# Kernel optimization log

Hardware: AMD Instinct MI355X
Metric: run time of the kernel (lower is better)

The kernel has to match this reference:

```python
import jax, jax.numpy as jnp
import numpy as np

N = 100000   # nodes
E = 600000   # edges
G = 4096     # graphs in batch
D_IN = 73
D_E = 101
D = 128      # latent_dim
BN_EPS = 1e-5


def _bn(h, gamma, beta):
    # BatchNorm1d in training mode: batch statistics (biased variance)
    m = h.mean(axis=0)
    v = h.var(axis=0)
    return (h - m) * jax.lax.rsqrt(v + BN_EPS) * gamma + beta


def setup_inputs() -> dict:
    key = jax.random.key(0)
    ks = jax.random.split(key, 24)
    inp = {
        "x": jax.random.normal(ks[0], (N, D_IN), jnp.float32),
        "edge_attr": jax.random.normal(ks[1], (E, D_E), jnp.float32),
        "src": jax.random.randint(ks[2], (E,), 0, N, jnp.int32),
        "dst": jax.random.randint(ks[3], (E,), 0, N, jnp.int32),
        "batch": jnp.sort(jax.random.randint(ks[4], (N,), 0, G, jnp.int32)),
        # node embedding Linear(73 -> 128)
        "W_emb": jax.random.normal(ks[5], (D_IN, D), jnp.float32) / np.sqrt(D_IN),
        "b_emb": jnp.zeros((D,), jnp.float32),
    }
    k = 6
    for i in range(2):
        inp[f"We{i}"] = jax.random.normal(ks[k], (D_E, D), jnp.float32) / np.sqrt(D_E); k += 1
        inp[f"be{i}"] = jnp.zeros((D,), jnp.float32)
        inp[f"W1_{i}"] = jax.random.normal(ks[k], (D, 2 * D), jnp.float32) / np.sqrt(D); k += 1
        inp[f"b1_{i}"] = jnp.zeros((2 * D,), jnp.float32)
        inp[f"g1_{i}"] = jnp.ones((2 * D,), jnp.float32)
        inp[f"bb1_{i}"] = jnp.zeros((2 * D,), jnp.float32)
        inp[f"W2_{i}"] = jax.random.normal(ks[k], (2 * D, D), jnp.float32) / np.sqrt(2 * D); k += 1
        inp[f"b2_{i}"] = jnp.zeros((D,), jnp.float32)
        inp[f"go_{i}"] = jnp.ones((D,), jnp.float32)
        inp[f"bo_{i}"] = jnp.zeros((D,), jnp.float32)
    return inp


def _forward(x, edge_attr, src, dst, batch,
             W_emb, b_emb,
             We0, be0, W1_0, b1_0, g1_0, bb1_0, W2_0, b2_0, go_0, bo_0,
             We1, be1, W1_1, b1_1, g1_1, bb1_1, W2_1, b2_1, go_1, bo_1):
    layers = [
        (We0, be0, W1_0, b1_0, g1_0, bb1_0, W2_0, b2_0, go_0, bo_0),
        (We1, be1, W1_1, b1_1, g1_1, bb1_1, W2_1, b2_1, go_1, bo_1),
    ]
    h = x @ W_emb + b_emb  # [N, D]
    n_layers = len(layers)
    for i, (We, be, W1, b1, g1, bb1, W2, b2, go, bo) in enumerate(layers):
        e = edge_attr @ We + be                         # [E, D]
        msg = jax.nn.relu(h[src] + e)                   # gather + add + ReLU
        agg = jax.ops.segment_sum(msg, dst, num_segments=N)  # scatter-sum
        z = h + agg                                     # (1 + eps) * x_i + aggr, eps = 0
        z = jax.nn.relu(_bn(z @ W1 + b1, g1, bb1))      # MLP: Linear -> BN -> ReLU
        h = _bn(z @ W2 + b2, go, bo)                    # Linear -> outer BN
        if i != n_layers - 1:
            h = jax.nn.relu(h)
        # dropout p=0 -> identity
    # global mean pool over graphs
    sums = jax.ops.segment_sum(h, batch, num_segments=G)            # [G, D]
    counts = jax.ops.segment_sum(jnp.ones((h.shape[0],), h.dtype), batch, num_segments=G)
    return sums / jnp.maximum(counts, 1.0)[:, None]


def reference(x, edge_attr, src, dst, batch,
              W_emb, b_emb,
              We0, be0, W1_0, b1_0, g1_0, bb1_0, W2_0, b2_0, go_0, bo_0,
              We1, be1, W1_1, b1_1, g1_1, bb1_1, W2_1, b2_1, go_1, bo_1):
    return _forward(x, edge_attr, src, dst, batch, W_emb, b_emb,
                    We0, be0, W1_0, b1_0, g1_0, bb1_0, W2_0, b2_0, go_0, bo_0,
                    We1, be1, W1_1, b1_1, g1_1, bb1_1, W2_1, b2_1, go_1, bo_1)
```

## Files before the change

### kernel.cpp

```cpp
#include <hip/hip_runtime.h>
#include <cstddef>

#define NN  100000
#define NE  600000
#define NG  4096
#define DIN 73
#define DE  101
#define DD  128
#define DD2 256
#define NP  100096
#define EP  600064

typedef unsigned int uint;
typedef unsigned short ushort;
typedef __attribute__((ext_vector_type(8))) short bf16x8;
typedef __attribute__((ext_vector_type(4))) float f32x4;

__device__ __forceinline__ void fadd_atomic(float* p, float v) { unsafeAtomicAdd(p, v); }

__device__ __forceinline__ ushort f2bf(float f) {
    uint u = __float_as_uint(f);
    uint r = (u + 0x7fffu + ((u >> 16) & 1u)) >> 16;
    return (ushort)r;
}
__device__ __forceinline__ float bf2f(ushort u) { return __uint_as_float(((uint)u) << 16); }


__global__ void hist_kernel(const int* __restrict__ dst, int* __restrict__ deg) {
    int e = blockIdx.x * blockDim.x + threadIdx.x;
    if (e < NE) atomicAdd(&deg[dst[e]], 1);
}

__global__ __launch_bounds__(256) void scan_chunk_kernel(
    const int* __restrict__ deg, int* __restrict__ offs, int* __restrict__ csums)
{
    const int b = blockIdx.x, t = threadIdx.x;
    const int base = b * 1024 + t * 4;
    int v[4];
    #pragma unroll
    for (int i = 0; i < 4; ++i) v[i] = (base + i < NN) ? deg[base + i] : 0;
    int tsum = v[0] + v[1] + v[2] + v[3];
    const int lane = t & 63, w = t >> 6;
    int x = tsum;
    #pragma unroll
    for (int d = 1; d < 64; d <<= 1) {
        int y = __shfl_up(x, d, 64);
        if (lane >= d) x += y;
    }
    __shared__ int wsum[4];
    if (lane == 63) wsum[w] = x;
    __syncthreads();
    int woff = 0;
    for (int i = 0; i < w; ++i) woff += wsum[i];
    int run = woff + x - tsum;
    #pragma unroll
    for (int i = 0; i < 4; ++i) {
        if (base + i < NN) offs[base + i] = run;
        run += v[i];
    }
    if (t == 255) csums[b] = woff + x;
}

__global__ void scan_tops_kernel(int* __restrict__ csums, int* __restrict__ offs, int nchunks) {
    if (threadIdx.x == 0 && blockIdx.x == 0) {
        int run = 0;
        for (int i = 0; i < nchunks; ++i) { int c = csums[i]; csums[i] = run; run += c; }
        offs[NN] = run;
    }
}

__global__ void scan_add_kernel(int* __restrict__ offs, const int* __restrict__ csums) {
    int i = blockIdx.x * blockDim.x + threadIdx.x;
    if (i < NN) offs[i] += csums[i >> 10];
}

__global__ void scatter_kernel(const int* __restrict__ dst, const int* __restrict__ offs,
                               int* __restrict__ cursor, int* __restrict__ csr)
{
    int e = blockIdx.x * blockDim.x + threadIdx.x;
    if (e >= NE) return;
    int d = dst[e];
    int pos = offs[d] + atomicAdd(&cursor[d], 1);
    csr[pos] = e;
}

__global__ void gstart_kernel(const int* __restrict__ batch, int* __restrict__ gstart) {
    int n = blockIdx.x * blockDim.x + threadIdx.x;
    if (n > NN) return;
    if (n == NN) {
        for (int g = batch[NN - 1] + 1; g <= NG; ++g) gstart[g] = NN;
        return;
    }
    int b = batch[n];
    int pb = (n == 0) ? -1 : batch[n - 1];
    for (int g = pb + 1; g <= b; ++g) gstart[g] = n;
}


__global__ __launch_bounds__(256) void cvt_ea_kernel(const float* __restrict__ ea,
                                                     ushort* __restrict__ eab)
{
    const int t = threadIdx.x;
    const int r = blockIdx.x * 8 + (t >> 5);
    if (r >= NE) return;
    const int c = (t & 31) * 4;
    ushort4 o;
    o.x = (c + 0 < DE) ? f2bf(ea[(size_t)r * DE + c + 0]) : (ushort)0;
    o.y = (c + 1 < DE) ? f2bf(ea[(size_t)r * DE + c + 1]) : (ushort)0;
    o.z = (c + 2 < DE) ? f2bf(ea[(size_t)r * DE + c + 2]) : (ushort)0;
    o.w = (c + 3 < DE) ? f2bf(ea[(size_t)r * DE + c + 3]) : (ushort)0;
    *(ushort4*)&eab[(size_t)r * 128 + c] = o;
}

__global__ void cvt_wt_kernel(const float* __restrict__ in, ushort* __restrict__ out,
                              int Kin, int Nn, int Kp)
{
    const int n = blockIdx.x;
    for (int k = threadIdx.x; k < Kp; k += blockDim.x)
        out[(size_t)n * Kp + k] = (k < Kin) ? f2bf(in[(size_t)k * Nn + n]) : (ushort)0;
}

template<int K>
__device__ __forceinline__ void mma_core(const ushort* __restrict__ Wt,
                                         const ushort* __restrict__ X,
                                         int n0, int m0, f32x4 acc[4][8])
{
    const int lane = threadIdx.x & 63;
    const int l15 = lane & 15, grp = lane >> 4;
    const size_t aoff = (size_t)(n0 + l15) * K + grp * 8;
    const size_t boff = (size_t)(m0 + l15) * K + grp * 8;
    #pragma unroll
    for (int kk = 0; kk < K / 32; ++kk) {
        bf16x8 a[8], b[4];
        #pragma unroll
        for (int nf = 0; nf < 8; ++nf)
            a[nf] = *(const bf16x8*)(Wt + aoff + (size_t)nf * 16 * K + kk * 32);
        #pragma unroll
        for (int mf = 0; mf < 4; ++mf)
            b[mf] = *(const bf16x8*)(X + boff + (size_t)mf * 16 * K + kk * 32);
        #pragma unroll
        for (int mf = 0; mf < 4; ++mf)
            #pragma unroll
            for (int nf = 0; nf < 8; ++nf)
                acc[mf][nf] = __builtin_amdgcn_mfma_f32_16x16x32_bf16(a[nf], b[mf], acc[mf][nf], 0, 0, 0);
    }
}

__device__ __forceinline__ void acc_zero(f32x4 acc[4][8]) {
    #pragma unroll
    for (int i = 0; i < 4; ++i)
        #pragma unroll
        for (int j = 0; j < 8; ++j)
            acc[i][j] = (f32x4){0.f, 0.f, 0.f, 0.f};
}

__global__ __launch_bounds__(256) void edge_gemm_kernel(
    const ushort* __restrict__ eab, const ushort* __restrict__ Wt,
    const float* __restrict__ be, const int* __restrict__ src,
    const float* __restrict__ h, ushort* __restrict__ msg)
{
    f32x4 acc[4][8];
    acc_zero(acc);
    const int e0 = blockIdx.x * 256 + (threadIdx.x >> 6) * 64;
    mma_core<128>(Wt, eab, 0, e0, acc);
    const int lane = threadIdx.x & 63, l15 = lane & 15, grp = lane >> 4;
    float4 bev[8];
    #pragma unroll
    for (int nf = 0; nf < 8; ++nf) bev[nf] = *(const float4*)&be[nf * 16 + grp * 4];
    #pragma unroll
    for (int mf = 0; mf < 4; ++mf) {
        const int e = e0 + mf * 16 + l15;
        const int sn = src[min(e, NE - 1)];
        const float* hp = &h[(size_t)sn * 128];
        #pragma unroll
        for (int nf = 0; nf < 8; ++nf) {
            const int nb = nf * 16 + grp * 4;
            const float4 hv = *(const float4*)&hp[nb];
            ushort4 o;
            o.x = f2bf(fmaxf(acc[mf][nf][0] + bev[nf].x + hv.x, 0.f));
            o.y = f2bf(fmaxf(acc[mf][nf][1] + bev[nf].y + hv.y, 0.f));
            o.z = f2bf(fmaxf(acc[mf][nf][2] + bev[nf].z + hv.z, 0.f));
            o.w = f2bf(fmaxf(acc[mf][nf][3] + bev[nf].w + hv.w, 0.f));
            *(ushort4*)&msg[(size_t)e * 128 + nb] = o;
        }
    }
}

__global__ __launch_bounds__(256) void mlp1_gemm_kernel(
    const ushort* __restrict__ z, const ushort* __restrict__ Wt,
    const float* __restrict__ bias, ushort* __restrict__ y)
{
    f32x4 acc[4][8];
    acc_zero(acc);
    const int m0 = blockIdx.x * 256 + (threadIdx.x >> 6) * 64;
    const int n0 = blockIdx.y * 128;
    mma_core<128>(Wt, z, n0, m0, acc);
    const int lane = threadIdx.x & 63, l15 = lane & 15, grp = lane >> 4;
    #pragma unroll
    for (int nf = 0; nf < 8; ++nf) {
        const int nb = n0 + nf * 16 + grp * 4;
        const float4 bv = *(const float4*)&bias[nb];
        #pragma unroll
        for (int mf = 0; mf < 4; ++mf) {
            const size_t m = m0 + mf * 16 + l15;
            ushort4 o;
            o.x = f2bf(acc[mf][nf][0] + bv.x);
            o.y = f2bf(acc[mf][nf][1] + bv.y);
            o.z = f2bf(acc[mf][nf][2] + bv.z);
            o.w = f2bf(acc[mf][nf][3] + bv.w);
            *(ushort4*)&y[m * 256 + nb] = o;
        }
    }
}

__global__ __launch_bounds__(256) void mlp2_gemm_kernel(
    const ushort* __restrict__ y1, const ushort* __restrict__ Wt,
    const float* __restrict__ bias, float* __restrict__ y2)
{
    f32x4 acc[4][8];
    acc_zero(acc);
    const int m0 = blockIdx.x * 256 + (threadIdx.x >> 6) * 64;
    mma_core<256>(Wt, y1, 0, m0, acc);
    const int lane = threadIdx.x & 63, l15 = lane & 15, grp = lane >> 4;
    #pragma unroll
    for (int nf = 0; nf < 8; ++nf) {
        const int nb = nf * 16 + grp * 4;
        const float4 bv = *(const float4*)&bias[nb];
        #pragma unroll
        for (int mf = 0; mf < 4; ++mf) {
            const size_t m = m0 + mf * 16 + l15;
            float4 o;
            o.x = acc[mf][nf][0] + bv.x;
            o.y = acc[mf][nf][1] + bv.y;
            o.z = acc[mf][nf][2] + bv.z;
            o.w = acc[mf][nf][3] + bv.w;
            *(float4*)&y2[m * 128 + nb] = o;
        }
    }
}


__global__ __launch_bounds__(128) void embed_kernel(
    const float* __restrict__ x, const float* __restrict__ W,
    const float* __restrict__ b, float* __restrict__ h)
{
    __shared__ float xs[4][DIN];
    const int n0 = blockIdx.x * 4;
    const int d  = threadIdx.x;
    for (int idx = d; idx < 4 * DIN; idx += 128) {
        int r = idx / DIN, c = idx - r * DIN;
        xs[r][c] = x[(size_t)n0 * DIN + idx];
    }
    __syncthreads();
    float bb = b[d];
    float a0 = bb, a1 = bb, a2 = bb, a3 = bb;
    for (int k = 0; k < DIN; ++k) {
        float w = W[k * DD + d];
        a0 = fmaf(xs[0][k], w, a0);
        a1 = fmaf(xs[1][k], w, a1);
        a2 = fmaf(xs[2][k], w, a2);
        a3 = fmaf(xs[3][k], w, a3);
    }
    h[(size_t)(n0 + 0) * DD + d] = a0;
    h[(size_t)(n0 + 1) * DD + d] = a1;
    h[(size_t)(n0 + 2) * DD + d] = a2;
    h[(size_t)(n0 + 3) * DD + d] = a3;
}

__global__ __launch_bounds__(256) void agg_kernel(
    const int* __restrict__ offs, const int* __restrict__ csr,
    const ushort* __restrict__ msgb, const float* __restrict__ h,
    ushort* __restrict__ zb)
{
    const int n = blockIdx.x * 4 + (threadIdx.x >> 6);
    if (n >= NN) return;
    const int lane = threadIdx.x & 63;
    const int s = offs[n], t = offs[n + 1];
    float a0 = 0.f, a1 = 0.f;
    for (int i = s; i < t; ++i) {
        const int e = csr[i];
        const uint mv = *(const uint*)&msgb[(size_t)e * 128 + lane * 2];
        a0 += __uint_as_float(mv << 16);
        a1 += __uint_as_float(mv & 0xffff0000u);
    }
    const float2 hv = *(const float2*)&h[(size_t)n * 128 + lane * 2];
    ushort2 o;
    o.x = f2bf(hv.x + a0);
    o.y = f2bf(hv.y + a1);
    *(ushort2*)&zb[(size_t)n * 128 + lane * 2] = o;
}

__global__ __launch_bounds__(256) void colstats256_kernel(
    const ushort* __restrict__ y, float* __restrict__ s, float* __restrict__ q)
{
    const int t = threadIdx.x;
    const int cs = (t & 63) * 4, rg = t >> 6;
    const int r0 = blockIdx.x * 256;
    float ps0 = 0, ps1 = 0, ps2 = 0, ps3 = 0, pq0 = 0, pq1 = 0, pq2 = 0, pq3 = 0;
    for (int i = rg; i < 256; i += 4) {
        const int r = r0 + i;
        if (r >= NN) break;
        ushort4 u = *(const ushort4*)&y[(size_t)r * 256 + cs];
        float f0 = bf2f(u.x), f1 = bf2f(u.y), f2v = bf2f(u.z), f3 = bf2f(u.w);
        ps0 += f0; pq0 += f0 * f0;
        ps1 += f1; pq1 += f1 * f1;
        ps2 += f2v; pq2 += f2v * f2v;
        ps3 += f3; pq3 += f3 * f3;
    }
    __shared__ float SS[4][256], SQ[4][256];
    SS[rg][cs + 0] = ps0; SS[rg][cs + 1] = ps1; SS[rg][cs + 2] = ps2; SS[rg][cs + 3] = ps3;
    SQ[rg][cs + 0] = pq0; SQ[rg][cs + 1] = pq1; SQ[rg][cs + 2] = pq2; SQ[rg][cs + 3] = pq3;
    __syncthreads();
    if (rg == 0) {
        #pragma unroll
        for (int j = 0; j < 4; ++j) {
            const int c = cs + j;
            fadd_atomic(&s[c], SS[0][c] + SS[1][c] + SS[2][c] + SS[3][c]);
            fadd_atomic(&q[c], SQ[0][c] + SQ[1][c] + SQ[2][c] + SQ[3][c]);
        }
    }
}

__global__ __launch_bounds__(256) void colstats128_kernel(
    const float* __restrict__ y, float* __restrict__ s, float* __restrict__ q)
{
    const int t = threadIdx.x;
    const int cs = (t & 31) * 4, rg = t >> 5;
    const int r0 = blockIdx.x * 256;
    float ps0 = 0, ps1 = 0, ps2 = 0, ps3 = 0, pq0 = 0, pq1 = 0, pq2 = 0, pq3 = 0;
    for (int i = rg; i < 256; i += 8) {
        const int r = r0 + i;
        if (r >= NN) break;
        float4 v = *(const float4*)&y[(size_t)r * 128 + cs];
        ps0 += v.x; pq0 += v.x * v.x;
        ps1 += v.y; pq1 += v.y * v.y;
        ps2 += v.z; pq2 += v.z * v.z;
        ps3 += v.w; pq3 += v.w * v.w;
    }
    __shared__ float SS[8][128], SQ[8][128];
    SS[rg][cs + 0] = ps0; SS[rg][cs + 1] = ps1; SS[rg][cs + 2] = ps2; SS[rg][cs + 3] = ps3;
    SQ[rg][cs + 0] = pq0; SQ[rg][cs + 1] = pq1; SQ[rg][cs + 2] = pq2; SQ[rg][cs + 3] = pq3;
    __syncthreads();
    if (rg == 0) {
        #pragma unroll
        for (int j = 0; j < 4; ++j) {
            const int c = cs + j;
            float sv = 0, qv = 0;
            #pragma unroll
            for (int g = 0; g < 8; ++g) { sv += SS[g][c]; qv += SQ[g][c]; }
            fadd_atomic(&s[c], sv);
            fadd_atomic(&q[c], qv);
        }
    }
}

__global__ void finalize_kernel(const float* __restrict__ s, const float* __restrict__ sq,
                                const float* __restrict__ g, const float* __restrict__ bb,
                                float* __restrict__ a, float* __restrict__ c,
                                int dim, float invN)
{
    int d = blockIdx.x * blockDim.x + threadIdx.x;
    if (d >= dim) return;
    float m  = s[d] * invN;
    float v  = sq[d] * invN - m * m;
    float rs = rsqrtf(v + 1e-5f);
    float ai = g[d] * rs;
    a[d] = ai;
    c[d] = bb[d] - m * ai;
}

__global__ void bnrelu_bf_kernel(ushort* __restrict__ y, const float* __restrict__ a,
                                 const float* __restrict__ c)
{
    int i = blockIdx.x * blockDim.x + threadIdx.x;
    const int stride = gridDim.x * blockDim.x;
    for (; i < NN * 64; i += stride) {
        const int cb = (i & 63) * 4;
        ushort4 u = *(const ushort4*)&y[(size_t)i * 4];
        const float4 av = *(const float4*)&a[cb];
        const float4 cv = *(const float4*)&c[cb];
        ushort4 o;
        o.x = f2bf(fmaxf(fmaf(bf2f(u.x), av.x, cv.x), 0.f));
        o.y = f2bf(fmaxf(fmaf(bf2f(u.y), av.y, cv.y), 0.f));
        o.z = f2bf(fmaxf(fmaf(bf2f(u.z), av.z, cv.z), 0.f));
        o.w = f2bf(fmaxf(fmaf(bf2f(u.w), av.w, cv.w), 0.f));
        *(ushort4*)&y[(size_t)i * 4] = o;
    }
}

__global__ void bn_relu_kernel(float* __restrict__ y2h, const float* __restrict__ a2,
                               const float* __restrict__ c2, int n4)
{
    int i = blockIdx.x * blockDim.x + threadIdx.x;
    const int stride = gridDim.x * blockDim.x;
    float4* p = (float4*)y2h;
    for (; i < n4; i += stride) {
        float4 v = p[i];
        const int d0 = (i & 31) * 4;
        v.x = fmaxf(fmaf(v.x, a2[d0 + 0], c2[d0 + 0]), 0.f);
        v.y = fmaxf(fmaf(v.y, a2[d0 + 1], c2[d0 + 1]), 0.f);
        v.z = fmaxf(fmaf(v.z, a2[d0 + 2], c2[d0 + 2]), 0.f);
        v.w = fmaxf(fmaf(v.w, a2[d0 + 3], c2[d0 + 3]), 0.f);
        p[i] = v;
    }
}

__global__ __launch_bounds__(256) void pool_kernel(
    const float* __restrict__ y2, const float* __restrict__ a2, const float* __restrict__ c2,
    const int* __restrict__ gstart, float* __restrict__ out)
{
    const int g = blockIdx.x * 4 + (threadIdx.x >> 6);
    if (g >= NG) return;
    const int lane = threadIdx.x & 63;
    const int s = gstart[g], t = gstart[g + 1];
    float a0 = 0.f, a1 = 0.f;
    for (int n = s; n < t; ++n) {
        const float2 v = *(const float2*)&y2[(size_t)n * 128 + lane * 2];
        a0 += v.x; a1 += v.y;
    }
    const int d0 = lane * 2;
    float2 o;
    if (t > s) {
        const float inv = 1.0f / (float)(t - s);
        o.x = fmaf(a2[d0 + 0], a0 * inv, c2[d0 + 0]);
        o.y = fmaf(a2[d0 + 1], a1 * inv, c2[d0 + 1]);
    } else {
        o.x = 0.f; o.y = 0.f;
    }
    *(float2*)&out[(size_t)g * 128 + d0] = o;
}


extern "C" void kernel_launch(void* const* d_in, const int* in_sizes, int n_in,
                              void* d_out, int out_size, void* d_ws, size_t ws_size,
                              hipStream_t stream)
{
    (void)in_sizes; (void)n_in; (void)out_size; (void)ws_size;
    const float* x     = (const float*)d_in[0];
    const float* ea    = (const float*)d_in[1];
    const int*   src   = (const int*)d_in[2];
    const int*   dst   = (const int*)d_in[3];
    const int*   batch = (const int*)d_in[4];
    const float* W_emb = (const float*)d_in[5];
    const float* b_emb = (const float*)d_in[6];

    char* ws = (char*)d_ws;
    auto alloc = [&](size_t bytes) { void* p = ws; ws += (bytes + 255) & ~(size_t)255; return p; };

    float*  hbuf = (float*) alloc((size_t)NP * 128 * 4);
    ushort* zb   = (ushort*)alloc((size_t)NP * 128 * 2);
    ushort* eab  = (ushort*)alloc((size_t)EP * 128 * 2);
    ushort* big  = (ushort*)alloc((size_t)EP * 128 * 2);
    ushort* msgb = big;
    ushort* y1b  = big;
    int* deg    = (int*)alloc((size_t)NN * 4);
    int* offs   = (int*)alloc((size_t)(NN + 1) * 4);
    int* csr    = (int*)alloc((size_t)NE * 4);
    int* csums  = (int*)alloc(128 * 4);
    int* gstart = (int*)alloc((size_t)(NG + 1) * 4);
    ushort* Wet[2], *W1t[2], *W2t[2];
    for (int l = 0; l < 2; ++l) {
        Wet[l] = (ushort*)alloc(128 * 128 * 2);
        W1t[l] = (ushort*)alloc(256 * 128 * 2);
        W2t[l] = (ushort*)alloc(128 * 256 * 2);
    }
    float* st = (float*)alloc(2048 * 4);
    float* s1 = st,        *sq1 = st + 256, *a1 = st + 512,  *c1 = st + 768;
    float* s2 = st + 1024, *sq2 = st + 1152, *a2 = st + 1280, *c2 = st + 1408;
    float* out = (float*)d_out;

    const int NCHUNK = (NN + 1023) / 1024;

    hipMemsetAsync(deg, 0, (size_t)NN * 4, stream);
    hist_kernel<<<(NE + 255) / 256, 256, 0, stream>>>(dst, deg);
    scan_chunk_kernel<<<NCHUNK, 256, 0, stream>>>(deg, offs, csums);
    scan_tops_kernel<<<1, 1, 0, stream>>>(csums, offs, NCHUNK);
    scan_add_kernel<<<(NN + 255) / 256, 256, 0, stream>>>(offs, csums);
    hipMemsetAsync(deg, 0, (size_t)NN * 4, stream);
    scatter_kernel<<<(NE + 255) / 256, 256, 0, stream>>>(dst, offs, deg, csr);
    gstart_kernel<<<(NN + 256) / 256, 256, 0, stream>>>(batch, gstart);

    cvt_ea_kernel<<<(NE + 7) / 8, 256, 0, stream>>>(ea, eab);
    for (int l = 0; l < 2; ++l) {
        const float* const* L = (const float* const*)(d_in + 7 + l * 10);
        cvt_wt_kernel<<<128, 128, 0, stream>>>(L[0], Wet[l], 101, 128, 128);
        cvt_wt_kernel<<<256, 128, 0, stream>>>(L[2], W1t[l], 128, 256, 128);
        cvt_wt_kernel<<<128, 128, 0, stream>>>(L[6], W2t[l], 256, 128, 256);
    }

    embed_kernel<<<NN / 4, 128, 0, stream>>>(x, W_emb, b_emb, hbuf);

    for (int layer = 0; layer < 2; ++layer) {
        const float* const* L = (const float* const*)(d_in + 7 + layer * 10);
        const float* be  = L[1];
        const float* b1  = L[3];
        const float* g1  = L[4]; const float* bb1 = L[5];
        const float* b2  = L[7];
        const float* go  = L[8]; const float* bo  = L[9];

        edge_gemm_kernel<<<EP / 256, 256, 0, stream>>>(eab, Wet[layer], be, src, hbuf, msgb);
        agg_kernel<<<NN / 4, 256, 0, stream>>>(offs, csr, msgb, hbuf, zb);

        hipMemsetAsync(s1, 0, 512 * sizeof(float), stream);
        hipMemsetAsync(s2, 0, 256 * sizeof(float), stream);

        mlp1_gemm_kernel<<<dim3(NP / 256, 2), 256, 0, stream>>>(zb, W1t[layer], b1, y1b);
        colstats256_kernel<<<NP / 256, 256, 0, stream>>>(y1b, s1, sq1);
        finalize_kernel<<<1, 256, 0, stream>>>(s1, sq1, g1, bb1, a1, c1, 256, 1.0f / NN);
        bnrelu_bf_kernel<<<2048, 256, 0, stream>>>(y1b, a1, c1);
        mlp2_gemm_kernel<<<NP / 256, 256, 0, stream>>>(y1b, W2t[layer], b2, hbuf);
        colstats128_kernel<<<NP / 256, 256, 0, stream>>>(hbuf, s2, sq2);
        finalize_kernel<<<1, 128, 0, stream>>>(s2, sq2, go, bo, a2, c2, 128, 1.0f / NN);

        if (layer == 0) {
            bn_relu_kernel<<<2048, 256, 0, stream>>>(hbuf, a2, c2, NN * 128 / 4);
        } else {
            pool_kernel<<<NG / 4, 256, 0, stream>>>(hbuf, a2, c2, gstart, out);
        }
    }
}
```

Measured before the change: 1.228 ms.

## Store edge projections in CSR order and keep node features in bf16

The edge GEMM now writes its bias-added projection directly at the edge's CSR position, found through a precomputed permutation. The aggregation kernel then streams those rows contiguously, gathers the source node row (via a permuted src array) and applies the add+ReLU itself, instead of doing a random gather in the GEMM epilogue and an indirect edge read in the aggregation. Node features h are also kept in bf16 throughout (embed, mlp2 output, BN/ReLU, colstats, pool), which halves node-feature traffic. The cost is extra bf16 rounding of h and a scattered write pattern in the edge GEMM epilogue.

```diff
diff --git a/kernel.cpp b/kernel.cpp
--- a/kernel.cpp
+++ b/kernel.cpp
@@ -74,14 +74,16 @@
     if (i < NN) offs[i] += csums[i >> 10];
 }
 
-__global__ void scatter_kernel(const int* __restrict__ dst, const int* __restrict__ offs,
-                               int* __restrict__ cursor, int* __restrict__ csr)
+__global__ void scatter_kernel(const int* __restrict__ dst, const int* __restrict__ src,
+                               const int* __restrict__ offs, int* __restrict__ cursor,
+                               int* __restrict__ eperm, int* __restrict__ srcp)
 {
     int e = blockIdx.x * blockDim.x + threadIdx.x;
     if (e >= NE) return;
     int d = dst[e];
     int pos = offs[d] + atomicAdd(&cursor[d], 1);
-    csr[pos] = e;
+    eperm[e] = pos;
+    srcp[pos] = src[e];
 }
 
 __global__ void gstart_kernel(const int* __restrict__ batch, int* __restrict__ gstart) {
@@ -102,13 +104,15 @@
 {
     const int t = threadIdx.x;
     const int r = blockIdx.x * 8 + (t >> 5);
-    if (r >= NE) return;
+    if (r >= EP) return;
     const int c = (t & 31) * 4;
-    ushort4 o;
-    o.x = (c + 0 < DE) ? f2bf(ea[(size_t)r * DE + c + 0]) : (ushort)0;
-    o.y = (c + 1 < DE) ? f2bf(ea[(size_t)r * DE + c + 1]) : (ushort)0;
-    o.z = (c + 2 < DE) ? f2bf(ea[(size_t)r * DE + c + 2]) : (ushort)0;
-    o.w = (c + 3 < DE) ? f2bf(ea[(size_t)r * DE + c + 3]) : (ushort)0;
+    ushort4 o = {0, 0, 0, 0};
+    if (r < NE) {
+        o.x = (c + 0 < DE) ? f2bf(ea[(size_t)r * DE + c + 0]) : (ushort)0;
+        o.y = (c + 1 < DE) ? f2bf(ea[(size_t)r * DE + c + 1]) : (ushort)0;
+        o.z = (c + 2 < DE) ? f2bf(ea[(size_t)r * DE + c + 2]) : (ushort)0;
+        o.w = (c + 3 < DE) ? f2bf(ea[(size_t)r * DE + c + 3]) : (ushort)0;
+    }
     *(ushort4*)&eab[(size_t)r * 128 + c] = o;
 }
 
@@ -156,34 +160,62 @@
 
 __global__ __launch_bounds__(256) void edge_gemm_kernel(
     const ushort* __restrict__ eab, const ushort* __restrict__ Wt,
-    const float* __restrict__ be, const int* __restrict__ src,
-    const float* __restrict__ h, ushort* __restrict__ msg)
-{
+    const float* __restrict__ be, const int* __restrict__ eperm,
+    ushort* __restrict__ ecsr)
+{
+    const int e0 = blockIdx.x * 256 + (threadIdx.x >> 6) * 64;
+    const int lane = threadIdx.x & 63, l15 = lane & 15, grp = lane >> 4;
+    int pos[4];
+    #pragma unroll
+    for (int mf = 0; mf < 4; ++mf) {
+        const int e = e0 + mf * 16 + l15;
+        pos[mf] = (e < NE) ? eperm[e] : -1;
+    }
     f32x4 acc[4][8];
     acc_zero(acc);
-    const int e0 = blockIdx.x * 256 + (threadIdx.x >> 6) * 64;
     mma_core<128>(Wt, eab, 0, e0, acc);
-    const int lane = threadIdx.x & 63, l15 = lane & 15, grp = lane >> 4;
     float4 bev[8];
     #pragma unroll
     for (int nf = 0; nf < 8; ++nf) bev[nf] = *(const float4*)&be[nf * 16 + grp * 4];
     #pragma unroll
     for (int mf = 0; mf < 4; ++mf) {
-        const int e = e0 + mf * 16 + l15;
-        const int sn = src[min(e, NE - 1)];
-        const float* hp = &h[(size_t)sn * 128];
+        if (pos[mf] < 0) continue;
+        ushort* rp = &ecsr[(size_t)pos[mf] * 128];
         #pragma unroll
         for (int nf = 0; nf < 8; ++nf) {
             const int nb = nf * 16 + grp * 4;
-            const float4 hv = *(const float4*)&hp[nb];
             ushort4 o;
-            o.x = f2bf(fmaxf(acc[mf][nf][0] + bev[nf].x + hv.x, 0.f));
-            o.y = f2bf(fmaxf(acc[mf][nf][1] + bev[nf].y + hv.y, 0.f));
-            o.z = f2bf(fmaxf(acc[mf][nf][2] + bev[nf].z + hv.z, 0.f));
-            o.w = f2bf(fmaxf(acc[mf][nf][3] + bev[nf].w + hv.w, 0.f));
-            *(ushort4*)&msg[(size_t)e * 128 + nb] = o;
+            o.x = f2bf(acc[mf][nf][0] + bev[nf].x);
+            o.y = f2bf(acc[mf][nf][1] + bev[nf].y);
+            o.z = f2bf(acc[mf][nf][2] + bev[nf].z);
+            o.w = f2bf(acc[mf][nf][3] + bev[nf].w);
+            *(ushort4*)&rp[nb] = o;
         }
     }
+}
+
+__global__ __launch_bounds__(256) void agg_kernel(
+    const int* __restrict__ offs, const int* __restrict__ srcp,
+    const ushort* __restrict__ ecsr, const ushort* __restrict__ hb,
+    ushort* __restrict__ zb)
+{
+    const int n = blockIdx.x * 4 + (threadIdx.x >> 6);
+    if (n >= NN) return;
+    const int lane = threadIdx.x & 63;
+    const int s = offs[n], t = offs[n + 1];
+    float a0 = 0.f, a1 = 0.f;
+    for (int i = s; i < t; ++i) {
+        const int sp = srcp[i];
+        const uint ev = *(const uint*)&ecsr[(size_t)i * 128 + lane * 2];
+        const uint hv = *(const uint*)&hb[(size_t)sp * 128 + lane * 2];
+        a0 += fmaxf(__uint_as_float(ev << 16) + __uint_as_float(hv << 16), 0.f);
+        a1 += fmaxf(__uint_as_float(ev & 0xffff0000u) + __uint_as_float(hv & 0xffff0000u), 0.f);
+    }
+    const uint hh = *(const uint*)&hb[(size_t)n * 128 + lane * 2];
+    ushort2 o;
+    o.x = f2bf(__uint_as_float(hh << 16) + a0);
+    o.y = f2bf(__uint_as_float(hh & 0xffff0000u) + a1);
+    *(ushort2*)&zb[(size_t)n * 128 + lane * 2] = o;
 }
 
 __global__ __launch_bounds__(256) void mlp1_gemm_kernel(
@@ -215,7 +247,7 @@
 
 __global__ __launch_bounds__(256) void mlp2_gemm_kernel(
     const ushort* __restrict__ y1, const ushort* __restrict__ Wt,
-    const float* __restrict__ bias, float* __restrict__ y2)
+    const float* __restrict__ bias, ushort* __restrict__ y2)
 {
     f32x4 acc[4][8];
     acc_zero(acc);
@@ -229,12 +261,12 @@
         #pragma unroll
         for (int mf = 0; mf < 4; ++mf) {
             const size_t m = m0 + mf * 16 + l15;
-            float4 o;
-            o.x = acc[mf][nf][0] + bv.x;
-            o.y = acc[mf][nf][1] + bv.y;
-            o.z = acc[mf][nf][2] + bv.z;
-            o.w = acc[mf][nf][3] + bv.w;
-            *(float4*)&y2[m * 128 + nb] = o;
+            ushort4 o;
+            o.x = f2bf(acc[mf][nf][0] + bv.x);
+            o.y = f2bf(acc[mf][nf][1] + bv.y);
+            o.z = f2bf(acc[mf][nf][2] + bv.z);
+            o.w = f2bf(acc[mf][nf][3] + bv.w);
+            *(ushort4*)&y2[m * 128 + nb] = o;
         }
     }
 }
@@ -242,7 +274,7 @@
 
 __global__ __launch_bounds__(128) void embed_kernel(
     const float* __restrict__ x, const float* __restrict__ W,
-    const float* __restrict__ b, float* __restrict__ h)
+    const float* __restrict__ b, ushort* __restrict__ hb)
 {
     __shared__ float xs[4][DIN];
     const int n0 = blockIdx.x * 4;
@@ -261,33 +293,10 @@
         a2 = fmaf(xs[2][k], w, a2);
         a3 = fmaf(xs[3][k], w, a3);
     }
-    h[(size_t)(n0 + 0) * DD + d] = a0;
-    h[(size_t)(n0 + 1) * DD + d] = a1;
-    h[(size_t)(n0 + 2) * DD + d] = a2;
-    h[(size_t)(n0 + 3) * DD + d] = a3;
-}
-
-__global__ __launch_bounds__(256) void agg_kernel(
-    const int* __restrict__ offs, const int* __restrict__ csr,
-    const ushort* __restrict__ msgb, const float* __restrict__ h,
-    ushort* __restrict__ zb)
-{
-    const int n = blockIdx.x * 4 + (threadIdx.x >> 6);
-    if (n >= NN) return;
-    const int lane = threadIdx.x & 63;
-    const int s = offs[n], t = offs[n + 1];
-    float a0 = 0.f, a1 = 0.f;
-    for (int i = s; i < t; ++i) {
-        const int e = csr[i];
-        const uint mv = *(const uint*)&msgb[(size_t)e * 128 + lane * 2];
-        a0 += __uint_as_float(mv << 16);
-        a1 += __uint_as_float(mv & 0xffff0000u);
-    }
-    const float2 hv = *(const float2*)&h[(size_t)n * 128 + lane * 2];
-    ushort2 o;
-    o.x = f2bf(hv.x + a0);
-    o.y = f2bf(hv.y + a1);
-    *(ushort2*)&zb[(size_t)n * 128 + lane * 2] = o;
+    hb[(size_t)(n0 + 0) * DD + d] = f2bf(a0);
+    hb[(size_t)(n0 + 1) * DD + d] = f2bf(a1);
+    hb[(size_t)(n0 + 2) * DD + d] = f2bf(a2);
+    hb[(size_t)(n0 + 3) * DD + d] = f2bf(a3);
 }
 
 __global__ __launch_bounds__(256) void colstats256_kernel(
@@ -321,8 +330,8 @@
     }
 }
 
-__global__ __launch_bounds__(256) void colstats128_kernel(
-    const float* __restrict__ y, float* __restrict__ s, float* __restrict__ q)
+__global__ __launch_bounds__(256) void colstats128b_kernel(
+    const ushort* __restrict__ y, float* __restrict__ s, float* __restrict__ q)
 {
     const int t = threadIdx.x;
     const int cs = (t & 31) * 4, rg = t >> 5;
@@ -331,11 +340,12 @@
     for (int i = rg; i < 256; i += 8) {
         const int r = r0 + i;
         if (r >= NN) break;
-        float4 v = *(const float4*)&y[(size_t)r * 128 + cs];
-        ps0 += v.x; pq0 += v.x * v.x;
-        ps1 += v.y; pq1 += v.y * v.y;
-        ps2 += v.z; pq2 += v.z * v.z;
-        ps3 += v.w; pq3 += v.w * v.w;
+        ushort4 u = *(const ushort4*)&y[(size_t)r * 128 + cs];
+        float f0 = bf2f(u.x), f1 = bf2f(u.y), f2v = bf2f(u.z), f3 = bf2f(u.w);
+        ps0 += f0; pq0 += f0 * f0;
+        ps1 += f1; pq1 += f1 * f1;
+        ps2 += f2v; pq2 += f2v * f2v;
+        ps3 += f3; pq3 += f3 * f3;
     }
     __shared__ float SS[8][128], SQ[8][128];
     SS[rg][cs + 0] = ps0; SS[rg][cs + 1] = ps1; SS[rg][cs + 2] = ps2; SS[rg][cs + 3] = ps3;
@@ -388,25 +398,27 @@
     }
 }
 
-__global__ void bn_relu_kernel(float* __restrict__ y2h, const float* __restrict__ a2,
-                               const float* __restrict__ c2, int n4)
+__global__ void bnrelu_hb_kernel(ushort* __restrict__ hb, const float* __restrict__ a,
+                                 const float* __restrict__ c)
 {
     int i = blockIdx.x * blockDim.x + threadIdx.x;
     const int stride = gridDim.x * blockDim.x;
-    float4* p = (float4*)y2h;
-    for (; i < n4; i += stride) {
-        float4 v = p[i];
-        const int d0 = (i & 31) * 4;
-        v.x = fmaxf(fmaf(v.x, a2[d0 + 0], c2[d0 + 0]), 0.f);
-        v.y = fmaxf(fmaf(v.y, a2[d0 + 1], c2[d0 + 1]), 0.f);
-        v.z = fmaxf(fmaf(v.z, a2[d0 + 2], c2[d0 + 2]), 0.f);
-        v.w = fmaxf(fmaf(v.w, a2[d0 + 3], c2[d0 + 3]), 0.f);
-        p[i] = v;
+    for (; i < NN * 32; i += stride) {
+        const int cb = (i & 31) * 4;
+        ushort4 u = *(const ushort4*)&hb[(size_t)i * 4];
+        const float4 av = *(const float4*)&a[cb];
+        const float4 cv = *(const float4*)&c[cb];
+        ushort4 o;
+        o.x = f2bf(fmaxf(fmaf(bf2f(u.x), av.x, cv.x), 0.f));
+        o.y = f2bf(fmaxf(fmaf(bf2f(u.y), av.y, cv.y), 0.f));
+        o.z = f2bf(fmaxf(fmaf(bf2f(u.z), av.z, cv.z), 0.f));
+        o.w = f2bf(fmaxf(fmaf(bf2f(u.w), av.w, cv.w), 0.f));
+        *(ushort4*)&hb[(size_t)i * 4] = o;
     }
 }
 
 __global__ __launch_bounds__(256) void pool_kernel(
-    const float* __restrict__ y2, const float* __restrict__ a2, const float* __restrict__ c2,
+    const ushort* __restrict__ hb, const float* __restrict__ a2, const float* __restrict__ c2,
     const int* __restrict__ gstart, float* __restrict__ out)
 {
     const int g = blockIdx.x * 4 + (threadIdx.x >> 6);
@@ -415,8 +427,9 @@
     const int s = gstart[g], t = gstart[g + 1];
     float a0 = 0.f, a1 = 0.f;
     for (int n = s; n < t; ++n) {
-        const float2 v = *(const float2*)&y2[(size_t)n * 128 + lane * 2];
-        a0 += v.x; a1 += v.y;
+        const uint v = *(const uint*)&hb[(size_t)n * 128 + lane * 2];
+        a0 += __uint_as_float(v << 16);
+        a1 += __uint_as_float(v & 0xffff0000u);
     }
     const int d0 = lane * 2;
     float2 o;
@@ -447,15 +460,16 @@
     char* ws = (char*)d_ws;
     auto alloc = [&](size_t bytes) { void* p = ws; ws += (bytes + 255) & ~(size_t)255; return p; };
 
-    float*  hbuf = (float*) alloc((size_t)NP * 128 * 4);
-    ushort* zb   = (ushort*)alloc((size_t)NP * 128 * 2);
-    ushort* eab  = (ushort*)alloc((size_t)EP * 128 * 2);
-    ushort* big  = (ushort*)alloc((size_t)EP * 128 * 2);
-    ushort* msgb = big;
+    ushort* hb  = (ushort*)alloc((size_t)NP * 128 * 2);
+    ushort* zb  = (ushort*)alloc((size_t)NP * 128 * 2);
+    ushort* eab = (ushort*)alloc((size_t)EP * 128 * 2);
+    ushort* big = (ushort*)alloc((size_t)EP * 128 * 2);
+    ushort* ecsr = big;
     ushort* y1b  = big;
     int* deg    = (int*)alloc((size_t)NN * 4);
     int* offs   = (int*)alloc((size_t)(NN + 1) * 4);
-    int* csr    = (int*)alloc((size_t)NE * 4);
+    int* eperm  = (int*)alloc((size_t)NE * 4);
+    int* srcp   = (int*)alloc((size_t)NE * 4);
     int* csums  = (int*)alloc(128 * 4);
     int* gstart = (int*)alloc((size_t)(NG + 1) * 4);
     ushort* Wet[2], *W1t[2], *W2t[2];
@@ -477,10 +491,10 @@
     scan_tops_kernel<<<1, 1, 0, stream>>>(csums, offs, NCHUNK);
     scan_add_kernel<<<(NN + 255) / 256, 256, 0, stream>>>(offs, csums);
     hipMemsetAsync(deg, 0, (size_t)NN * 4, stream);
-    scatter_kernel<<<(NE + 255) / 256, 256, 0, stream>>>(dst, offs, deg, csr);
+    scatter_kernel<<<(NE + 255) / 256, 256, 0, stream>>>(dst, src, offs, deg, eperm, srcp);
     gstart_kernel<<<(NN + 256) / 256, 256, 0, stream>>>(batch, gstart);
 
-    cvt_ea_kernel<<<(NE + 7) / 8, 256, 0, stream>>>(ea, eab);
+    cvt_ea_kernel<<<EP / 8, 256, 0, stream>>>(ea, eab);
     for (int l = 0; l < 2; ++l) {
         const float* const* L = (const float* const*)(d_in + 7 + l * 10);
         cvt_wt_kernel<<<128, 128, 0, stream>>>(L[0], Wet[l], 101, 128, 128);
@@ -488,7 +502,7 @@
         cvt_wt_kernel<<<128, 128, 0, stream>>>(L[6], W2t[l], 256, 128, 256);
     }
 
-    embed_kernel<<<NN / 4, 128, 0, stream>>>(x, W_emb, b_emb, hbuf);
+    embed_kernel<<<NN / 4, 128, 0, stream>>>(x, W_emb, b_emb, hb);
 
     for (int layer = 0; layer < 2; ++layer) {
         const float* const* L = (const float* const*)(d_in + 7 + layer * 10);
@@ -498,8 +512,8 @@
         const float* b2  = L[7];
         const float* go  = L[8]; const float* bo  = L[9];
 
-        edge_gemm_kernel<<<EP / 256, 256, 0, stream>>>(eab, Wet[layer], be, src, hbuf, msgb);
-        agg_kernel<<<NN / 4, 256, 0, stream>>>(offs, csr, msgb, hbuf, zb);
+        edge_gemm_kernel<<<EP / 256, 256, 0, stream>>>(eab, Wet[layer], be, eperm, ecsr);
+        agg_kernel<<<NN / 4, 256, 0, stream>>>(offs, srcp, ecsr, hb, zb);
 
         hipMemsetAsync(s1, 0, 512 * sizeof(float), stream);
         hipMemsetAsync(s2, 0, 256 * sizeof(float), stream);
@@ -508,14 +522,14 @@
         colstats256_kernel<<<NP / 256, 256, 0, stream>>>(y1b, s1, sq1);
         finalize_kernel<<<1, 256, 0, stream>>>(s1, sq1, g1, bb1, a1, c1, 256, 1.0f / NN);
         bnrelu_bf_kernel<<<2048, 256, 0, stream>>>(y1b, a1, c1);
-        mlp2_gemm_kernel<<<NP / 256, 256, 0, stream>>>(y1b, W2t[layer], b2, hbuf);
-        colstats128_kernel<<<NP / 256, 256, 0, stream>>>(hbuf, s2, sq2);
+        mlp2_gemm_kernel<<<NP / 256, 256, 0, stream>>>(y1b, W2t[layer], b2, hb);
+        colstats128b_kernel<<<NP / 256, 256, 0, stream>>>(hb, s2, sq2);
         finalize_kernel<<<1, 128, 0, stream>>>(s2, sq2, go, bo, a2, c2, 128, 1.0f / NN);
 
         if (layer == 0) {
-            bn_relu_kernel<<<2048, 256, 0, stream>>>(hbuf, a2, c2, NN * 128 / 4);
+            bnrelu_hb_kernel<<<2048, 256, 0, stream>>>(hb, a2, c2);
         } else {
-            pool_kernel<<<NG / 4, 256, 0, stream>>>(hbuf, a2, c2, gstart, out);
+            pool_kernel<<<NG / 4, 256, 0, stream>>>(hb, a2, c2, gstart, out);
         }
     }
 }
```

Result: faster. 1.149 ms (-6.4%).
